# Performance work log

Measured on AMD Instinct MI355X. Metric: run time of the kernel, lower is better.

The kernel has to match this reference:

```python
import jax, jax.numpy as jnp
import numpy as np

EPS = 1e-15


def _cost_matrix(height, width):
    # Mirrors torch: x=arange(width), y=arange(height), meshgrid (ij), cdist p=2.
    x = jnp.arange(width, dtype=jnp.float32)
    y = jnp.arange(height, dtype=jnp.float32)
    X, Y = jnp.meshgrid(x, y, indexing='ij')          # (W, H)
    coords = jnp.stack([X.ravel(), Y.ravel()], axis=1)  # (HW, 2)
    sq = jnp.sum(coords * coords, axis=1)
    d2 = sq[:, None] + sq[None, :] - 2.0 * (coords @ coords.T)
    return jnp.sqrt(jnp.maximum(d2, 0.0))             # (HW, HW)


def setup_inputs() -> dict:
    key = jax.random.key(0)
    B, C, H, W = 8, 5, 96, 96
    k1, k2 = jax.random.split(key)
    outputs = jax.random.normal(k1, (B, C, H, W), dtype=jnp.float32)
    targets = jax.random.randint(k2, (B, H, W), 0, C, dtype=jnp.int64)
    cost_matrix = _cost_matrix(H, W)
    return {"outputs": outputs, "targets": targets, "cost_matrix": cost_matrix}


def reference(outputs, targets, cost_matrix):
    B, C, H, W = outputs.shape
    N = H * W
    # one-hot target masks per class, flattened spatially: (B, C, N)
    onehot = (targets.reshape(B, 1, N) == jnp.arange(C)[None, :, None]).astype(outputs.dtype)
    pred = jnp.exp(outputs).reshape(B, C, N)
    t = onehot / (jnp.sum(onehot, axis=-1, keepdims=True) + EPS)
    p = pred / (jnp.sum(pred, axis=-1, keepdims=True) + EPS)
    # sum_{i,j} cost[i,j] * |t-p|[b,j]  ==  (sum_i cost[i,j]) . |t-p|[b,:]
    colsum = jnp.sum(cost_matrix, axis=0)             # (N,)
    wd = jnp.einsum('bcn,n->bc', jnp.abs(t - p), colsum)  # (B, C)
    # (1/C) * sum_cls mean_batch == mean over (B, C)
    return jnp.mean(wd)
```

## Files before the change

### kernel.cpp

```cpp
#include <hip/hip_runtime.h>
#include <math.h>

#define HW    96
#define N_PIX 9216
#define B_DIM 8
#define C_DIM 5
#define BC    (B_DIM * C_DIM)
#define EPS   1e-15f

__global__ void colsum_kernel(float* __restrict__ colsum) {
    __shared__ float smem[4];
    int j = blockIdx.x;
    float xj = (float)(j / HW);
    float yj = (float)(j % HW);

    float acc = 0.f;
    for (int i = threadIdx.x; i < N_PIX; i += 256) {
        float dx = (float)(i / HW) - xj;
        float dy = (float)(i % HW) - yj;
        acc += sqrtf(dx * dx + dy * dy);
    }
#pragma unroll
    for (int off = 32; off > 0; off >>= 1)
        acc += __shfl_down(acc, off, 64);
    int wave = threadIdx.x >> 6;
    int lane = threadIdx.x & 63;
    if (lane == 0) smem[wave] = acc;
    __syncthreads();
    if (threadIdx.x == 0)
        colsum[j] = smem[0] + smem[1] + smem[2] + smem[3];
}

__global__ void __launch_bounds__(1024) wd_kernel(const float* __restrict__ outputs,
                                                  const int* __restrict__ targets,
                                                  const float* __restrict__ colsum,
                                                  float* __restrict__ out) {
    __shared__ float smem_a[16];
    __shared__ float smem_b[16];
    __shared__ float bcast[2];

    const int bc = blockIdx.x;
    const int b = bc / C_DIM, c = bc % C_DIM;
    const float* o  = outputs + (size_t)bc * N_PIX;
    const int*   tg = targets + (size_t)b  * N_PIX;

    const int K = N_PIX / 1024;
    float e[K], cs[K];
    int   hit[K];

    float es = 0.f, ct = 0.f;
#pragma unroll
    for (int k = 0; k < K; ++k) {
        int n = threadIdx.x + k * 1024;
        float v = expf(o[n]);
        e[k] = v; es += v;
        int h = (tg[n] == c) ? 1 : 0;
        hit[k] = h; ct += (float)h;
        cs[k] = colsum[n];
    }

#pragma unroll
    for (int off = 32; off > 0; off >>= 1) {
        es += __shfl_down(es, off, 64);
        ct += __shfl_down(ct, off, 64);
    }
    int wave = threadIdx.x >> 6;
    int lane = threadIdx.x & 63;
    if (lane == 0) { smem_a[wave] = es; smem_b[wave] = ct; }
    __syncthreads();
    if (threadIdx.x == 0) {
        float tes = 0.f, tct = 0.f;
#pragma unroll
        for (int w = 0; w < 16; ++w) { tes += smem_a[w]; tct += smem_b[w]; }
        bcast[0] = tes; bcast[1] = tct;
    }
    __syncthreads();

    const float inv_es = 1.f / (bcast[0] + EPS);
    const float inv_ct = 1.f / (bcast[1] + EPS);

    float acc = 0.f;
#pragma unroll
    for (int k = 0; k < K; ++k) {
        float p = e[k] * inv_es;
        float t = hit[k] ? inv_ct : 0.f;
        acc += cs[k] * fabsf(t - p);
    }
#pragma unroll
    for (int off = 32; off > 0; off >>= 1)
        acc += __shfl_down(acc, off, 64);
    if (lane == 0) smem_a[wave] = acc;
    __syncthreads();
    if (threadIdx.x == 0) {
        float tot = 0.f;
#pragma unroll
        for (int w = 0; w < 16; ++w) tot += smem_a[w];
        atomicAdd(out, tot * (1.f / (float)BC));
    }
}

extern "C" void kernel_launch(void* const* d_in, const int* in_sizes, int n_in,
                              void* d_out, int out_size, void* d_ws, size_t ws_size,
                              hipStream_t stream) {
    const float* outputs = (const float*)d_in[0];
    const int*   targets = (const int*)d_in[1];

    float* out    = (float*)d_out;
    float* colsum = (float*)d_ws;

    hipMemsetAsync(d_out, 0, sizeof(float), stream);

    colsum_kernel<<<N_PIX, 256, 0, stream>>>(colsum);
    wd_kernel<<<BC, 1024, 0, stream>>>(outputs, targets, colsum, out);
}
```

Baseline: 423.4 us.

## Exploit grid symmetry in colsum and fold output zeroing into kernel

The column-sum kernel now computes only one quadrant of pixels and writes each result to its four mirror-symmetric positions, cutting the sqrt work by four. Each block uses 384 threads laid out as 96 x-values by 4 row groups of 24 unrolled y-steps, which removes per-element integer division. The separate memset of the output is dropped and block 0 of the colsum kernel zeroes it instead, saving one stream operation. This relies on the wd kernel running strictly after the colsum kernel on the same stream.

```diff
diff --git a/kernel.cpp b/kernel.cpp
--- a/kernel.cpp
+++ b/kernel.cpp
@@ -8,27 +8,44 @@
 #define BC    (B_DIM * C_DIM)
 #define EPS   1e-15f
 
-__global__ void colsum_kernel(float* __restrict__ colsum) {
-    __shared__ float smem[4];
-    int j = blockIdx.x;
-    float xj = (float)(j / HW);
-    float yj = (float)(j % HW);
+__global__ void __launch_bounds__(384) colsum_kernel(float* __restrict__ colsum,
+                                                     float* __restrict__ out) {
+    __shared__ float smem[6];
+    const int bx = blockIdx.x;
+    const int xq = bx / 48;
+    const int yq = bx % 48;
+
+    const int t  = threadIdx.x;
+    const int xi = t % 96;
+    const int g  = t / 96;
+
+    const float dx   = (float)xi - (float)xq;
+    const float dxsq = dx * dx;
 
     float acc = 0.f;
-    for (int i = threadIdx.x; i < N_PIX; i += 256) {
-        float dx = (float)(i / HW) - xj;
-        float dy = (float)(i % HW) - yj;
-        acc += sqrtf(dx * dx + dy * dy);
+    float dy  = (float)(g * 24) - (float)yq;
+#pragma unroll
+    for (int k = 0; k < 24; ++k) {
+        acc += sqrtf(fmaf(dy, dy, dxsq));
+        dy += 1.f;
     }
+
 #pragma unroll
     for (int off = 32; off > 0; off >>= 1)
         acc += __shfl_down(acc, off, 64);
-    int wave = threadIdx.x >> 6;
-    int lane = threadIdx.x & 63;
+    const int wave = t >> 6;
+    const int lane = t & 63;
     if (lane == 0) smem[wave] = acc;
     __syncthreads();
-    if (threadIdx.x == 0)
-        colsum[j] = smem[0] + smem[1] + smem[2] + smem[3];
+    if (t == 0) {
+        float s = smem[0] + smem[1] + smem[2] + smem[3] + smem[4] + smem[5];
+        const int xm = 95 - xq, ym = 95 - yq;
+        colsum[xq * HW + yq] = s;
+        colsum[xm * HW + yq] = s;
+        colsum[xq * HW + ym] = s;
+        colsum[xm * HW + ym] = s;
+        if (bx == 0) *out = 0.f;
+    }
 }
 
 __global__ void __launch_bounds__(1024) wd_kernel(const float* __restrict__ outputs,
@@ -108,8 +125,6 @@
     float* out    = (float*)d_out;
     float* colsum = (float*)d_ws;
 
-    hipMemsetAsync(d_out, 0, sizeof(float), stream);
-
-    colsum_kernel<<<N_PIX, 256, 0, stream>>>(colsum);
+    colsum_kernel<<<48 * 48, 384, 0, stream>>>(colsum, out);
     wd_kernel<<<BC, 1024, 0, stream>>>(outputs, targets, colsum, out);
 }
```

Result: faster. 381.8 us (-9.8%).
